# Optimization experiments

Measured on AMD Instinct MI355X. Metric: run time of the kernel, lower is better.

The kernel has to match this reference:

```python
import jax, jax.numpy as jnp
import numpy as np

# MLA dims (DeepSeek-V2-Lite-class)
B, S, D = 2, 2048, 2048
H = 16
NOPE, ROPE, VD = 128, 64, 128   # qk_nope_head_dim, qk_rope_head_dim, v_head_dim
KV_RANK, Q_RANK = 512, 1536
EPS = 1e-6
THETA = 10000.0


def setup_inputs() -> dict:
    key = jax.random.key(0)
    ks = jax.random.split(key, 8)

    def init(k, shape, fan_in):
        return jax.random.normal(k, shape, jnp.float32) * (fan_in ** -0.5)

    return {
        "x": jax.random.normal(ks[0], (B, S, D), jnp.float32),
        "w_dq": init(ks[1], (D, Q_RANK), D),
        "q_a_norm": jnp.ones((Q_RANK,), jnp.float32),
        "w_uq": init(ks[2], (Q_RANK, H * (NOPE + ROPE)), Q_RANK),
        "w_dkv": init(ks[3], (D, KV_RANK + ROPE), D),
        "kv_a_norm": jnp.ones((KV_RANK,), jnp.float32),
        "w_ukv": init(ks[4], (KV_RANK, H * (NOPE + VD)), KV_RANK),
        "w_o": init(ks[5], (H * VD, D), H * VD),
    }


def _rmsnorm(x, w):
    return x * jax.lax.rsqrt(jnp.mean(x * x, axis=-1, keepdims=True) + EPS) * w


def _rope(x):
    # x: [B, S, H', d] -> rotary on last dim (half-split style)
    d = x.shape[-1]
    inv = 1.0 / (THETA ** (jnp.arange(0, d, 2, dtype=jnp.float32) / d))
    ang = jnp.arange(x.shape[1], dtype=jnp.float32)[:, None] * inv[None, :]  # [S, d/2]
    cos = jnp.cos(ang)[None, :, None, :]
    sin = jnp.sin(ang)[None, :, None, :]
    x1, x2 = jnp.split(x, 2, axis=-1)
    return jnp.concatenate([x1 * cos - x2 * sin, x2 * cos + x1 * sin], axis=-1)


def reference(x, w_dq, q_a_norm, w_uq, w_dkv, kv_a_norm, w_ukv, w_o):
    # --- low-rank Q projection ---
    q = _rmsnorm(x @ w_dq, q_a_norm) @ w_uq          # [B,S,H*(NOPE+ROPE)]
    q = q.reshape(B, S, H, NOPE + ROPE)
    q_nope, q_pe = q[..., :NOPE], q[..., NOPE:]

    # --- latent (compressed) KV projection + shared decoupled-RoPE key ---
    ckv = x @ w_dkv                                   # [B,S,KV_RANK+ROPE]
    c_kv, k_pe = ckv[..., :KV_RANK], ckv[..., KV_RANK:]
    kv = (_rmsnorm(c_kv, kv_a_norm) @ w_ukv).reshape(B, S, H, NOPE + VD)
    k_nope, v = kv[..., :NOPE], kv[..., NOPE:]

    # --- decoupled RoPE on rope dims only ---
    q_pe = _rope(q_pe)                                # [B,S,H,ROPE]
    k_pe = _rope(k_pe[:, :, None, :])                 # [B,S,1,ROPE] shared across heads

    qf = jnp.concatenate([q_nope, q_pe], axis=-1)     # [B,S,H,NOPE+ROPE]
    kf = jnp.concatenate([k_nope, jnp.broadcast_to(k_pe, (B, S, H, ROPE))], axis=-1)

    # --- scaled dot-product attention with causal mask ---
    scale = 1.0 / jnp.sqrt(jnp.float32(NOPE + ROPE))
    scores = jnp.einsum("bqhd,bkhd->bhqk", qf * scale, kf)  # [B,H,S,S]
    causal = jnp.tril(jnp.ones((S, S), bool))
    scores = jnp.where(causal[None, None], scores, -1e9)
    w = jax.nn.softmax(scores, axis=-1)
    o = jnp.einsum("bhqk,bkhd->bqhd", w, v).reshape(B, S, H * VD)
    return o @ w_o                                    # [B,S,D]
```

## Files before the change

kernel.cpp:

```cpp
#include <hip/hip_runtime.h>
#include <hip/hip_bf16.h>
#include <math.h>

#define SS 2048
#define HH 16
#define EPSF 1e-6f
#define MR 4096
#define L2T 13.287712379549449f
#define ASCL (0.07216878364870322f * 1.4426950408889634f)

typedef unsigned short u16;
typedef unsigned int u32;
typedef __attribute__((ext_vector_type(8))) short bf8_t;
typedef __attribute__((ext_vector_type(4))) float f4_t;

__device__ inline u16 f2b(float f) {
    __hip_bfloat16 h = __float2bfloat16(f);
    return __builtin_bit_cast(u16, h);
}
__device__ inline float b2f(u16 x) {
    u32 v = (u32)x << 16;
    return __builtin_bit_cast(float, v);
}

#define GLD16(g, l) __builtin_amdgcn_global_load_lds( \
    (const __attribute__((address_space(1))) u32*)(g), \
    (__attribute__((address_space(3))) u32*)(l), 16, 0, 0)

#define MFMA16(a,b,c) __builtin_amdgcn_mfma_f32_16x16x32_bf16((a),(b),(c),0,0,0)

__global__ void prep_k(const float* __restrict__ x, u16* __restrict__ xb,
                       const float* __restrict__ w_dq, const float* __restrict__ w_dkv,
                       const float* __restrict__ w_uq, const float* __restrict__ w_ukv,
                       const float* __restrict__ w_o,
                       u16* __restrict__ wT1, u16* __restrict__ wTuq,
                       u16* __restrict__ wTukv, u16* __restrict__ wTo) {
    __shared__ float tt[32][33];
    int blk = blockIdx.x, tid = threadIdx.x;
    if (blk < 8192) {
        int i = blk * 256 + tid;
        float4 v = ((const float4*)x)[i];
        ushort4 o;
        o.x = f2b(v.x); o.y = f2b(v.y); o.z = f2b(v.z); o.w = f2b(v.w);
        *(ushort4*)(xb + (size_t)i * 4) = o;
        return;
    }
    blk -= 8192;
    const float* W; u16* dst; int K, N, Npad, nx;
    if (blk < 3072)       { W = w_dq;  dst = wT1;                      K = 2048; N = 1536; Npad = 1536; nx = 48; }
    else if (blk < 4352)  { blk -= 3072; W = w_dkv; dst = wT1 + (size_t)1536 * 2048; K = 2048; N = 576;  Npad = 640;  nx = 20; }
    else if (blk < 8960)  { blk -= 4352; W = w_uq;  dst = wTuq;        K = 1536; N = 3072; Npad = 3072; nx = 96; }
    else if (blk < 11008) { blk -= 8960; W = w_ukv; dst = wTukv;       K = 512;  N = 4096; Npad = 4096; nx = 128; }
    else                  { blk -= 11008; W = w_o;  dst = wTo;         K = 2048; N = 2048; Npad = 2048; nx = 64; }
    int n0 = (blk % nx) * 32, k0 = (blk / nx) * 32;
    int tx = tid & 31, ty = tid >> 5;
    for (int i = ty; i < 32; i += 8) {
        int n = n0 + tx;
        tt[i][tx] = (n < N) ? W[(size_t)(k0 + i) * N + n] : 0.f;
    }
    __syncthreads();
    for (int i = ty; i < 32; i += 8) {
        int n = n0 + i;
        if (n < Npad) dst[(size_t)n * K + k0 + tx] = f2b(tt[tx][i]);
    }
}

template <int MODE>
__global__ __launch_bounds__(256, 2)
void gemm_mfma(const u16* __restrict__ A, const u16* __restrict__ BT,
               void* __restrict__ Cv, int K, int N) {
    __shared__ u16 lA[128 * 32];
    __shared__ u16 lB[128 * 32];
    const int tid = threadIdx.x;
    const int w = tid >> 6, lane = tid & 63;
    const int quad = lane >> 4, col = lane & 15;
    const int wm = (w >> 1) * 64, wn = (w & 1) * 64;
    const int bm = blockIdx.y * 128, bn = blockIdx.x * 128;
    const int srow = lane >> 2;
    const int scol = (lane & 3) * 8;
    f4_t acc[4][4] = {};
    for (int k0 = 0; k0 < K; k0 += 32) {
        __syncthreads();
        #pragma unroll
        for (int cc = 0; cc < 2; cc++) {
            int c = 2 * w + cc;
            int row = c * 16 + srow;
            GLD16(A  + (size_t)(bm + row) * K + k0 + scol, (char*)lA + c * 1024);
            GLD16(BT + (size_t)(bn + row) * K + k0 + scol, (char*)lB + c * 1024);
        }
        __syncthreads();
        bf8_t af[4], bf[4];
        #pragma unroll
        for (int i = 0; i < 4; i++) {
            af[i] = *(const bf8_t*)(lA + (wm + i * 16 + col) * 32 + quad * 8);
            bf[i] = *(const bf8_t*)(lB + (wn + i * 16 + col) * 32 + quad * 8);
        }
        #pragma unroll
        for (int mi = 0; mi < 4; mi++)
            #pragma unroll
            for (int ni = 0; ni < 4; ni++)
                acc[mi][ni] = MFMA16(af[mi], bf[ni], acc[mi][ni]);
    }
    if (MODE == 0) {
        float* C = (float*)Cv;
        #pragma unroll
        for (int mi = 0; mi < 4; mi++)
            #pragma unroll
            for (int ni = 0; ni < 4; ni++) {
                int n = bn + wn + ni * 16 + col;
                #pragma unroll
                for (int r = 0; r < 4; r++) {
                    int m = bm + wm + mi * 16 + quad * 4 + r;
                    C[(size_t)m * N + n] = acc[mi][ni][r];
                }
            }
    } else if (MODE == 1) {
        u16* C = (u16*)Cv;
        #pragma unroll
        for (int mi = 0; mi < 4; mi++)
            #pragma unroll
            for (int ni = 0; ni < 4; ni++) {
                int n = bn + wn + ni * 16 + col;
                #pragma unroll
                for (int r = 0; r < 4; r++) {
                    int m = bm + wm + mi * 16 + quad * 4 + r;
                    C[(size_t)m * N + n] = f2b(acc[mi][ni][r]);
                }
            }
    } else {
        u16* C = (u16*)Cv;
        int span = ((bn + wn) >> 6) % 3;
        if (span < 2) {
            #pragma unroll
            for (int mi = 0; mi < 4; mi++)
                #pragma unroll
                for (int ni = 0; ni < 4; ni++) {
                    int n = bn + wn + ni * 16 + col;
                    #pragma unroll
                    for (int r = 0; r < 4; r++) {
                        int m = bm + wm + mi * 16 + quad * 4 + r;
                        C[(size_t)m * N + n] = f2b(acc[mi][ni][r] * ASCL);
                    }
                }
        } else {
            #pragma unroll
            for (int ni = 0; ni < 2; ni++) {
                int e = ni * 16 + col;
                float inv = exp2f(-(float)e * (L2T / 32.0f));
                #pragma unroll
                for (int mi = 0; mi < 4; mi++) {
                    #pragma unroll
                    for (int r = 0; r < 4; r++) {
                        int m = bm + wm + mi * 16 + quad * 4 + r;
                        int pos = m & (SS - 1);
                        float ang = (float)pos * inv;
                        float cs, sn; sincosf(ang, &sn, &cs);
                        float x1 = acc[mi][ni][r], x2 = acc[mi][ni + 2][r];
                        int n = bn + wn + ni * 16 + col;
                        C[(size_t)m * N + n]      = f2b((x1 * cs - x2 * sn) * ASCL);
                        C[(size_t)m * N + n + 32] = f2b((x2 * cs + x1 * sn) * ASCL);
                    }
                }
            }
        }
    }
}

__global__ void rmsq_k(const u16* __restrict__ C1, const float* __restrict__ wt,
                       u16* __restrict__ qlb) {
    __shared__ float red[256];
    int row = blockIdx.x, tid = threadIdx.x;
    const ushort4* rp = (const ushort4*)(C1 + (size_t)row * 2176);
    float s = 0.f;
    for (int i = tid; i < 384; i += 256) {
        ushort4 u = rp[i];
        float a = b2f(u.x), b = b2f(u.y), c = b2f(u.z), d = b2f(u.w);
        s += a * a + b * b + c * c + d * d;
    }
    red[tid] = s;
    __syncthreads();
    for (int off = 128; off > 0; off >>= 1) {
        if (tid < off) red[tid] += red[tid + off];
        __syncthreads();
    }
    float sc = rsqrtf(red[0] * (1.0f / 1536.0f) + EPSF);
    ushort4* op = (ushort4*)(qlb + (size_t)row * 1536);
    const float4* wv = (const float4*)wt;
    for (int i = tid; i < 384; i += 256) {
        ushort4 u = rp[i];
        float4 ww = wv[i];
        ushort4 o;
        o.x = f2b(b2f(u.x) * sc * ww.x);
        o.y = f2b(b2f(u.y) * sc * ww.y);
        o.z = f2b(b2f(u.z) * sc * ww.z);
        o.w = f2b(b2f(u.w) * sc * ww.w);
        op[i] = o;
    }
}

__global__ void rmskv_rope_k(const u16* __restrict__ C1, const float* __restrict__ wt,
                             u16* __restrict__ ckvnb, u16* __restrict__ kpeb) {
    __shared__ float red[256];
    int row = blockIdx.x, tid = threadIdx.x;
    const u16* base = C1 + (size_t)row * 2176 + 1536;
    if (tid < 32) {
        int t = tid;
        float x1 = b2f(base[512 + t]), x2 = b2f(base[544 + t]);
        int pos = row & (SS - 1);
        float inv = exp2f(-(float)t * (L2T / 32.0f));
        float ang = (float)pos * inv;
        float cs, sn; sincosf(ang, &sn, &cs);
        kpeb[(size_t)row * 64 + t]      = f2b(x1 * cs - x2 * sn);
        kpeb[(size_t)row * 64 + 32 + t] = f2b(x2 * cs + x1 * sn);
    }
    const ushort4* rp = (const ushort4*)base;
    float s = 0.f;
    if (tid < 128) {
        ushort4 u = rp[tid];
        float a = b2f(u.x), b = b2f(u.y), c = b2f(u.z), d = b2f(u.w);
        s = a * a + b * b + c * c + d * d;
    }
    red[tid] = s;
    __syncthreads();
    for (int off = 128; off > 0; off >>= 1) {
        if (tid < off) red[tid] += red[tid + off];
        __syncthreads();
    }
    float sc = rsqrtf(red[0] * (1.0f / 512.0f) + EPSF);
    if (tid < 128) {
        ushort4 u = rp[tid];
        float4 ww = ((const float4*)wt)[tid];
        ushort4 o;
        o.x = f2b(b2f(u.x) * sc * ww.x);
        o.y = f2b(b2f(u.y) * sc * ww.y);
        o.z = f2b(b2f(u.z) * sc * ww.z);
        o.w = f2b(b2f(u.w) * sc * ww.w);
        ((ushort4*)(ckvnb + (size_t)row * 512))[tid] = o;
    }
}

__global__ __launch_bounds__(256, 3)
void attn_mfma(const u16* __restrict__ qb, const u16* __restrict__ kvb,
               const u16* __restrict__ kpe, u16* __restrict__ ob) {
    __shared__ u16 lK[64 * 200];
    __shared__ u16 lV[128 * 72];
    __shared__ u16 lP[4 * 16 * 80];
    const int tid = threadIdx.x, w = tid >> 6, lane = tid & 63;
    const int quad = lane >> 4, col = lane & 15;
    const int bh = blockIdx.x, b = bh >> 4, h = bh & 15;
    const int tok0 = b * SS;
    int offE[7], isKV[7];
    #pragma unroll
    for (int jj = 0; jj < 7; jj++) {
        int c = w + 4 * jj;
        int o_b = c * 1024 + lane * 16;
        int row = o_b / 400;
        int ro = o_b - row * 400;
        if (ro < 256)      { offE[jj] = (row * 16 + h) * 256 + (ro >> 1); isKV[jj] = 1; }
        else if (ro < 384) { offE[jj] = row * 64 + ((ro - 256) >> 1);     isKV[jj] = 0; }
        else               { offE[jj] = 0;                                 isKV[jj] = 0; }
    }
    const int kp2 = lane & 31, dh = lane >> 5;
    u16* pw = lP + w * 16 * 80;

    for (int ph = 0; ph < 2; ph++) {
        const int qt = ph ? (31 - (int)blockIdx.y) : (int)blockIdx.y;
        bf8_t qf[6];
        {
            int qtok = tok0 + qt * 64 + w * 16 + col;
            const u16* qp = qb + ((size_t)qtok * HH + h) * 192 + quad * 8;
            #pragma unroll
            for (int kc = 0; kc < 6; kc++) qf[kc] = *(const bf8_t*)(qp + kc * 32);
        }
        f4_t o[8] = {};
        float mrow[4] = {-1e30f, -1e30f, -1e30f, -1e30f};
        float lrow[4] = {0.f, 0.f, 0.f, 0.f};
        for (int kt = 0; kt <= qt; kt++) {
            int ktok = tok0 + kt * 64;
            __syncthreads();
            #pragma unroll
            for (int jj = 0; jj < 7; jj++) {
                int c = w + 4 * jj;
                if (c < 25) {
                    const u16* src = isKV[jj] ? kvb + (size_t)ktok * 4096 + offE[jj]
                                              : kpe + (size_t)ktok * 64   + offE[jj];
                    GLD16(src, (char*)lK + c * 1024);
                }
            }
            #pragma unroll
            for (int i = 0; i < 2; i++) {
                int dv8 = w * 4 + dh * 2 + i;
                const u16* v0 = kvb + ((size_t)(ktok + 2 * kp2) * HH + h) * 256 + 128 + dv8 * 8;
                uint4 a4 = *(const uint4*)v0;
                uint4 b4 = *(const uint4*)(v0 + 4096);
                u32 av[4] = {a4.x, a4.y, a4.z, a4.w};
                u32 bv[4] = {b4.x, b4.y, b4.z, b4.w};
                u32* dst = (u32*)lV + (size_t)(dv8 * 8) * 36 + kp2;
                #pragma unroll
                for (int t = 0; t < 4; t++) {
                    u32 lo = __builtin_amdgcn_perm(bv[t], av[t], 0x05040100u);
                    u32 hi = __builtin_amdgcn_perm(bv[t], av[t], 0x07060302u);
                    dst[(2 * t) * 36]     = lo;
                    dst[(2 * t + 1) * 36] = hi;
                }
            }
            __syncthreads();
            bool diag = (kt == qt);
            f4_t s[4] = {};
            #pragma unroll
            for (int t = 0; t < 4; t++) {
                if (!diag || t <= w) {
                    #pragma unroll
                    for (int kc = 0; kc < 6; kc++) {
                        bf8_t kf = *(const bf8_t*)(lK + (t * 16 + col) * 200 + kc * 32 + quad * 8);
                        s[t] = MFMA16(qf[kc], kf, s[t]);
                    }
                }
            }
            if (diag) {
                #pragma unroll
                for (int t = 0; t < 4; t++) {
                    int kg = t * 16 + col;
                    #pragma unroll
                    for (int r = 0; r < 4; r++) {
                        int qg = w * 16 + quad * 4 + r;
                        if (kg > qg) s[t][r] = -1e30f;
                    }
                }
            }
            float sm[4] = {-1e30f, -1e30f, -1e30f, -1e30f};
            #pragma unroll
            for (int t = 0; t < 4; t++)
                #pragma unroll
                for (int r = 0; r < 4; r++) sm[r] = fmaxf(sm[r], s[t][r]);
            #pragma unroll
            for (int off = 1; off < 16; off <<= 1)
                #pragma unroll
                for (int r = 0; r < 4; r++) sm[r] = fmaxf(sm[r], __shfl_xor(sm[r], off));
            float al[4];
            #pragma unroll
            for (int r = 0; r < 4; r++) {
                float mn = fmaxf(mrow[r], sm[r]);
                al[r] = exp2f(mrow[r] - mn);
                mrow[r] = mn;
            }
            float rs[4] = {0.f, 0.f, 0.f, 0.f};
            #pragma unroll
            for (int t = 0; t < 4; t++)
                #pragma unroll
                for (int r = 0; r < 4; r++) {
                    float p = exp2f(s[t][r] - mrow[r]);
                    s[t][r] = p;
                    rs[r] += p;
                }
            #pragma unroll
            for (int off = 1; off < 16; off <<= 1)
                #pragma unroll
                for (int r = 0; r < 4; r++) rs[r] += __shfl_xor(rs[r], off);
            #pragma unroll
            for (int r = 0; r < 4; r++) lrow[r] = lrow[r] * al[r] + rs[r];
            #pragma unroll
            for (int n = 0; n < 8; n++)
                #pragma unroll
                for (int r = 0; r < 4; r++) o[n][r] *= al[r];
            #pragma unroll
            for (int t = 0; t < 4; t++)
                #pragma unroll
                for (int r = 0; r < 4; r++)
                    pw[(quad * 4 + r) * 80 + t * 16 + col] = f2b(s[t][r]);
            #pragma unroll
            for (int kc2 = 0; kc2 < 2; kc2++) {
                bf8_t pf = *(const bf8_t*)(pw + col * 80 + kc2 * 32 + quad * 8);
                #pragma unroll
                for (int n = 0; n < 8; n++) {
                    bf8_t vf = *(const bf8_t*)(lV + (n * 16 + col) * 72 + kc2 * 32 + quad * 8);
                    o[n] = MFMA16(pf, vf, o[n]);
                }
            }
        }
        #pragma unroll
        for (int n = 0; n < 8; n++)
            #pragma unroll
            for (int r = 0; r < 4; r++) {
                int qtok = tok0 + qt * 64 + w * 16 + quad * 4 + r;
                ob[((size_t)qtok * HH + h) * 128 + n * 16 + col] = f2b(o[n][r] / lrow[r]);
            }
    }
}

extern "C" void kernel_launch(void* const* d_in, const int* in_sizes, int n_in,
                              void* d_out, int out_size, void* d_ws, size_t ws_size,
                              hipStream_t stream) {
    const float* x        = (const float*)d_in[0];
    const float* w_dq     = (const float*)d_in[1];
    const float* q_a_norm = (const float*)d_in[2];
    const float* w_uq     = (const float*)d_in[3];
    const float* w_dkv    = (const float*)d_in[4];
    const float* kv_a_nrm = (const float*)d_in[5];
    const float* w_ukv    = (const float*)d_in[6];
    const float* w_o      = (const float*)d_in[7];
    float* out = (float*)d_out;

    char* ws = (char*)d_ws;
    const size_t MB = 1024 * 1024;
    u16* xb    = (u16*)(ws);
    u16* wT1   = (u16*)(ws + 17 * MB);
    u16* wTuq  = (u16*)(ws + 26 * MB);
    u16* wTukv = (u16*)(ws + 36 * MB);
    u16* wTo   = (u16*)(ws + 41 * MB);
    u16* C1    = (u16*)(ws + 50 * MB);
    u16* qlb   = (u16*)(ws + 68 * MB);
    u16* qbuf  = (u16*)(ws + 81 * MB);
    u16* ckvnb = (u16*)(ws + 106 * MB);
    u16* kpeb  = (u16*)(ws + 110 * MB);
    u16* kvb   = (u16*)(ws + 111 * MB);
    u16* aob   = xb;

    prep_k<<<23296, 256, 0, stream>>>(x, xb, w_dq, w_dkv, w_uq, w_ukv, w_o,
                                      wT1, wTuq, wTukv, wTo);
    gemm_mfma<1><<<dim3(17, 32), 256, 0, stream>>>(xb, wT1, C1, 2048, 2176);
    rmsq_k<<<MR, 256, 0, stream>>>(C1, q_a_norm, qlb);
    gemm_mfma<2><<<dim3(24, 32), 256, 0, stream>>>(qlb, wTuq, qbuf, 1536, 3072);
    rmskv_rope_k<<<MR, 256, 0, stream>>>(C1, kv_a_nrm, ckvnb, kpeb);
    gemm_mfma<1><<<dim3(32, 32), 256, 0, stream>>>(ckvnb, wTukv, kvb, 512, 4096);
    attn_mfma<<<dim3(32, 16), 256, 0, stream>>>(qbuf, kvb, kpeb, aob);
    gemm_mfma<0><<<dim3(16, 32), 256, 0, stream>>>(aob, wTo, out, 2048, 2048);
}
```

Before: 462.0 us.

## Restructure KV layout: head-major K with rope, transposed V, double-buffered attention

The up-projection GEMM epilogue now writes K as a per-token, per-head 192-wide buffer, with the shared rope key broadcast into it by a merged RMS-norm kernel. V is written transposed per head so attention can read V fragments straight from global memory into registers, with no LDS transpose. The attention kernel double-buffers K tiles in LDS, prefetching the next tile while computing the current one, and drops occupancy to 2. The two RMS kernels are merged into one launch and GEMM launch bounds are tuned per call; the cost is redundant K-rope storage and more global traffic for V.

```diff
diff --git a/kernel.cpp b/kernel.cpp
--- a/kernel.cpp
+++ b/kernel.cpp
@@ -65,10 +65,10 @@
     }
 }
 
-template <int MODE>
-__global__ __launch_bounds__(256, 2)
+template <int MODE, int MINW>
+__global__ __launch_bounds__(256, MINW)
 void gemm_mfma(const u16* __restrict__ A, const u16* __restrict__ BT,
-               void* __restrict__ Cv, int K, int N) {
+               void* __restrict__ Cv, void* __restrict__ Cv2, int K, int N) {
     __shared__ u16 lA[128 * 32];
     __shared__ u16 lB[128 * 32];
     const int tid = threadIdx.x;
@@ -127,7 +127,7 @@
                     C[(size_t)m * N + n] = f2b(acc[mi][ni][r]);
                 }
             }
-    } else {
+    } else if (MODE == 2) {
         u16* C = (u16*)Cv;
         int span = ((bn + wn) >> 6) % 3;
         if (span < 2) {
@@ -163,105 +163,138 @@
                 }
             }
         }
-    }
-}
-
-__global__ void rmsq_k(const u16* __restrict__ C1, const float* __restrict__ wt,
-                       u16* __restrict__ qlb) {
+    } else {
+        u16* kb = (u16*)Cv;
+        u16* vT = (u16*)Cv2;
+        #pragma unroll
+        for (int ni = 0; ni < 4; ni++) {
+            int nb = bn + wn + ni * 16;
+            int h = nb >> 8;
+            int cb = nb & 255;
+            if (cb < 128) {
+                #pragma unroll
+                for (int mi = 0; mi < 4; mi++)
+                    #pragma unroll
+                    for (int r = 0; r < 4; r++) {
+                        int m = bm + wm + mi * 16 + quad * 4 + r;
+                        kb[((size_t)m * HH + h) * 192 + cb + col] = f2b(acc[mi][ni][r]);
+                    }
+            } else {
+                int dv = cb - 128 + col;
+                #pragma unroll
+                for (int mi = 0; mi < 4; mi++) {
+                    int mb = bm + wm + mi * 16 + quad * 4;
+                    ushort4 o;
+                    o.x = f2b(acc[mi][ni][0]);
+                    o.y = f2b(acc[mi][ni][1]);
+                    o.z = f2b(acc[mi][ni][2]);
+                    o.w = f2b(acc[mi][ni][3]);
+                    *(ushort4*)(vT + ((size_t)h * 128 + dv) * 4096 + mb) = o;
+                }
+            }
+        }
+    }
+}
+
+__global__ void rms_all_k(const u16* __restrict__ C1, const float* __restrict__ wq,
+                          const float* __restrict__ wkv,
+                          u16* __restrict__ qlb, u16* __restrict__ ckvnb,
+                          u16* __restrict__ kb) {
     __shared__ float red[256];
-    int row = blockIdx.x, tid = threadIdx.x;
-    const ushort4* rp = (const ushort4*)(C1 + (size_t)row * 2176);
-    float s = 0.f;
-    for (int i = tid; i < 384; i += 256) {
-        ushort4 u = rp[i];
-        float a = b2f(u.x), b = b2f(u.y), c = b2f(u.z), d = b2f(u.w);
-        s += a * a + b * b + c * c + d * d;
-    }
-    red[tid] = s;
-    __syncthreads();
-    for (int off = 128; off > 0; off >>= 1) {
-        if (tid < off) red[tid] += red[tid + off];
+    int tid = threadIdx.x;
+    if (blockIdx.x < 4096) {
+        int row = blockIdx.x;
+        const ushort4* rp = (const ushort4*)(C1 + (size_t)row * 2176);
+        float s = 0.f;
+        for (int i = tid; i < 384; i += 256) {
+            ushort4 u = rp[i];
+            float a = b2f(u.x), b = b2f(u.y), c = b2f(u.z), d = b2f(u.w);
+            s += a * a + b * b + c * c + d * d;
+        }
+        red[tid] = s;
         __syncthreads();
-    }
-    float sc = rsqrtf(red[0] * (1.0f / 1536.0f) + EPSF);
-    ushort4* op = (ushort4*)(qlb + (size_t)row * 1536);
-    const float4* wv = (const float4*)wt;
-    for (int i = tid; i < 384; i += 256) {
-        ushort4 u = rp[i];
-        float4 ww = wv[i];
-        ushort4 o;
-        o.x = f2b(b2f(u.x) * sc * ww.x);
-        o.y = f2b(b2f(u.y) * sc * ww.y);
-        o.z = f2b(b2f(u.z) * sc * ww.z);
-        o.w = f2b(b2f(u.w) * sc * ww.w);
-        op[i] = o;
-    }
-}
-
-__global__ void rmskv_rope_k(const u16* __restrict__ C1, const float* __restrict__ wt,
-                             u16* __restrict__ ckvnb, u16* __restrict__ kpeb) {
-    __shared__ float red[256];
-    int row = blockIdx.x, tid = threadIdx.x;
-    const u16* base = C1 + (size_t)row * 2176 + 1536;
-    if (tid < 32) {
-        int t = tid;
-        float x1 = b2f(base[512 + t]), x2 = b2f(base[544 + t]);
-        int pos = row & (SS - 1);
-        float inv = exp2f(-(float)t * (L2T / 32.0f));
-        float ang = (float)pos * inv;
-        float cs, sn; sincosf(ang, &sn, &cs);
-        kpeb[(size_t)row * 64 + t]      = f2b(x1 * cs - x2 * sn);
-        kpeb[(size_t)row * 64 + 32 + t] = f2b(x2 * cs + x1 * sn);
-    }
-    const ushort4* rp = (const ushort4*)base;
-    float s = 0.f;
-    if (tid < 128) {
-        ushort4 u = rp[tid];
-        float a = b2f(u.x), b = b2f(u.y), c = b2f(u.z), d = b2f(u.w);
-        s = a * a + b * b + c * c + d * d;
-    }
-    red[tid] = s;
-    __syncthreads();
-    for (int off = 128; off > 0; off >>= 1) {
-        if (tid < off) red[tid] += red[tid + off];
+        for (int off = 128; off > 0; off >>= 1) {
+            if (tid < off) red[tid] += red[tid + off];
+            __syncthreads();
+        }
+        float sc = rsqrtf(red[0] * (1.0f / 1536.0f) + EPSF);
+        ushort4* op = (ushort4*)(qlb + (size_t)row * 1536);
+        const float4* wv = (const float4*)wq;
+        for (int i = tid; i < 384; i += 256) {
+            ushort4 u = rp[i];
+            float4 ww = wv[i];
+            ushort4 o;
+            o.x = f2b(b2f(u.x) * sc * ww.x);
+            o.y = f2b(b2f(u.y) * sc * ww.y);
+            o.z = f2b(b2f(u.z) * sc * ww.z);
+            o.w = f2b(b2f(u.w) * sc * ww.w);
+            op[i] = o;
+        }
+    } else {
+        int row = blockIdx.x - 4096;
+        const u16* base = C1 + (size_t)row * 2176 + 1536;
+        if (tid < 32) {
+            int t = tid;
+            float x1 = b2f(base[512 + t]), x2 = b2f(base[544 + t]);
+            int pos = row & (SS - 1);
+            float inv = exp2f(-(float)t * (L2T / 32.0f));
+            float ang = (float)pos * inv;
+            float cs, sn; sincosf(ang, &sn, &cs);
+            u16 y1 = f2b(x1 * cs - x2 * sn);
+            u16 y2 = f2b(x2 * cs + x1 * sn);
+            u16* kr = kb + (size_t)row * HH * 192;
+            #pragma unroll
+            for (int h = 0; h < HH; h++) {
+                kr[h * 192 + 128 + t] = y1;
+                kr[h * 192 + 160 + t] = y2;
+            }
+        }
+        const ushort4* rp = (const ushort4*)base;
+        float s = 0.f;
+        if (tid < 128) {
+            ushort4 u = rp[tid];
+            float a = b2f(u.x), b = b2f(u.y), c = b2f(u.z), d = b2f(u.w);
+            s = a * a + b * b + c * c + d * d;
+        }
+        red[tid] = s;
         __syncthreads();
-    }
-    float sc = rsqrtf(red[0] * (1.0f / 512.0f) + EPSF);
-    if (tid < 128) {
-        ushort4 u = rp[tid];
-        float4 ww = ((const float4*)wt)[tid];
-        ushort4 o;
-        o.x = f2b(b2f(u.x) * sc * ww.x);
-        o.y = f2b(b2f(u.y) * sc * ww.y);
-        o.z = f2b(b2f(u.z) * sc * ww.z);
-        o.w = f2b(b2f(u.w) * sc * ww.w);
-        ((ushort4*)(ckvnb + (size_t)row * 512))[tid] = o;
-    }
-}
-
-__global__ __launch_bounds__(256, 3)
-void attn_mfma(const u16* __restrict__ qb, const u16* __restrict__ kvb,
-               const u16* __restrict__ kpe, u16* __restrict__ ob) {
-    __shared__ u16 lK[64 * 200];
-    __shared__ u16 lV[128 * 72];
-    __shared__ u16 lP[4 * 16 * 80];
+        for (int off = 128; off > 0; off >>= 1) {
+            if (tid < off) red[tid] += red[tid + off];
+            __syncthreads();
+        }
+        float sc = rsqrtf(red[0] * (1.0f / 512.0f) + EPSF);
+        if (tid < 128) {
+            ushort4 u = rp[tid];
+            float4 ww = ((const float4*)wkv)[tid];
+            ushort4 o;
+            o.x = f2b(b2f(u.x) * sc * ww.x);
+            o.y = f2b(b2f(u.y) * sc * ww.y);
+            o.z = f2b(b2f(u.z) * sc * ww.z);
+            o.w = f2b(b2f(u.w) * sc * ww.w);
+            ((ushort4*)(ckvnb + (size_t)row * 512))[tid] = o;
+        }
+    }
+}
+
+__global__ __launch_bounds__(256, 2)
+void attn_mfma(const u16* __restrict__ qb, const u16* __restrict__ kb,
+               const u16* __restrict__ vT, u16* __restrict__ ob) {
+    __shared__ u16 lK[2][64 * 200];
+    __shared__ u16 lP[4 * 16 * 72];
     const int tid = threadIdx.x, w = tid >> 6, lane = tid & 63;
     const int quad = lane >> 4, col = lane & 15;
     const int bh = blockIdx.x, b = bh >> 4, h = bh & 15;
     const int tok0 = b * SS;
-    int offE[7], isKV[7];
+    int goff[7];
     #pragma unroll
     for (int jj = 0; jj < 7; jj++) {
         int c = w + 4 * jj;
         int o_b = c * 1024 + lane * 16;
         int row = o_b / 400;
         int ro = o_b - row * 400;
-        if (ro < 256)      { offE[jj] = (row * 16 + h) * 256 + (ro >> 1); isKV[jj] = 1; }
-        else if (ro < 384) { offE[jj] = row * 64 + ((ro - 256) >> 1);     isKV[jj] = 0; }
-        else               { offE[jj] = 0;                                 isKV[jj] = 0; }
-    }
-    const int kp2 = lane & 31, dh = lane >> 5;
-    u16* pw = lP + w * 16 * 80;
+        goff[jj] = (ro < 384) ? (row * HH + h) * 192 + (ro >> 1) : 0;
+    }
+    u16* pw = lP + w * 16 * 72;
 
     for (int ph = 0; ph < 2; ph++) {
         const int qt = ph ? (31 - (int)blockIdx.y) : (int)blockIdx.y;
@@ -275,36 +308,36 @@
         f4_t o[8] = {};
         float mrow[4] = {-1e30f, -1e30f, -1e30f, -1e30f};
         float lrow[4] = {0.f, 0.f, 0.f, 0.f};
-        for (int kt = 0; kt <= qt; kt++) {
-            int ktok = tok0 + kt * 64;
-            __syncthreads();
+        {
+            size_t kbase = (size_t)(tok0) * (HH * 192);
             #pragma unroll
             for (int jj = 0; jj < 7; jj++) {
                 int c = w + 4 * jj;
-                if (c < 25) {
-                    const u16* src = isKV[jj] ? kvb + (size_t)ktok * 4096 + offE[jj]
-                                              : kpe + (size_t)ktok * 64   + offE[jj];
-                    GLD16(src, (char*)lK + c * 1024);
-                }
-            }
-            #pragma unroll
-            for (int i = 0; i < 2; i++) {
-                int dv8 = w * 4 + dh * 2 + i;
-                const u16* v0 = kvb + ((size_t)(ktok + 2 * kp2) * HH + h) * 256 + 128 + dv8 * 8;
-                uint4 a4 = *(const uint4*)v0;
-                uint4 b4 = *(const uint4*)(v0 + 4096);
-                u32 av[4] = {a4.x, a4.y, a4.z, a4.w};
-                u32 bv[4] = {b4.x, b4.y, b4.z, b4.w};
-                u32* dst = (u32*)lV + (size_t)(dv8 * 8) * 36 + kp2;
-                #pragma unroll
-                for (int t = 0; t < 4; t++) {
-                    u32 lo = __builtin_amdgcn_perm(bv[t], av[t], 0x05040100u);
-                    u32 hi = __builtin_amdgcn_perm(bv[t], av[t], 0x07060302u);
-                    dst[(2 * t) * 36]     = lo;
-                    dst[(2 * t + 1) * 36] = hi;
-                }
-            }
-            __syncthreads();
+                if (c < 25) GLD16(kb + kbase + goff[jj], (char*)lK[0] + c * 1024);
+            }
+        }
+        __syncthreads();
+        for (int kt = 0; kt <= qt; kt++) {
+            const u16* cur = lK[kt & 1];
+            if (kt < qt) {
+                size_t kbase = (size_t)(tok0 + (kt + 1) * 64) * (HH * 192);
+                u16* nxt = (u16*)lK[(kt + 1) & 1];
+                #pragma unroll
+                for (int jj = 0; jj < 7; jj++) {
+                    int c = w + 4 * jj;
+                    if (c < 25) GLD16(kb + kbase + goff[jj], (char*)nxt + c * 1024);
+                }
+            }
+            bf8_t vf[2][8];
+            {
+                const u16* vbase = vT + (size_t)(h * 128 + col) * 4096
+                                 + tok0 + kt * 64 + quad * 8;
+                #pragma unroll
+                for (int kc2 = 0; kc2 < 2; kc2++)
+                    #pragma unroll
+                    for (int n = 0; n < 8; n++)
+                        vf[kc2][n] = *(const bf8_t*)(vbase + (size_t)(n * 16) * 4096 + kc2 * 32);
+            }
             bool diag = (kt == qt);
             f4_t s[4] = {};
             #pragma unroll
@@ -312,7 +345,7 @@
                 if (!diag || t <= w) {
                     #pragma unroll
                     for (int kc = 0; kc < 6; kc++) {
-                        bf8_t kf = *(const bf8_t*)(lK + (t * 16 + col) * 200 + kc * 32 + quad * 8);
+                        bf8_t kf = *(const bf8_t*)(cur + (t * 16 + col) * 200 + kc * 32 + quad * 8);
                         s[t] = MFMA16(qf[kc], kf, s[t]);
                     }
                 }
@@ -367,16 +400,15 @@
             for (int t = 0; t < 4; t++)
                 #pragma unroll
                 for (int r = 0; r < 4; r++)
-                    pw[(quad * 4 + r) * 80 + t * 16 + col] = f2b(s[t][r]);
+                    pw[(quad * 4 + r) * 72 + t * 16 + col] = f2b(s[t][r]);
             #pragma unroll
             for (int kc2 = 0; kc2 < 2; kc2++) {
-                bf8_t pf = *(const bf8_t*)(pw + col * 80 + kc2 * 32 + quad * 8);
-                #pragma unroll
-                for (int n = 0; n < 8; n++) {
-                    bf8_t vf = *(const bf8_t*)(lV + (n * 16 + col) * 72 + kc2 * 32 + quad * 8);
-                    o[n] = MFMA16(pf, vf, o[n]);
-                }
-            }
+                bf8_t pf = *(const bf8_t*)(pw + col * 72 + kc2 * 32 + quad * 8);
+                #pragma unroll
+                for (int n = 0; n < 8; n++)
+                    o[n] = MFMA16(pf, vf[kc2][n], o[n]);
+            }
+            __syncthreads();
         }
         #pragma unroll
         for (int n = 0; n < 8; n++)
@@ -411,18 +443,17 @@
     u16* C1    = (u16*)(ws + 50 * MB);
     u16* qlb   = (u16*)(ws + 68 * MB);
     u16* qbuf  = (u16*)(ws + 81 * MB);
-    u16* ckvnb = (u16*)(ws + 106 * MB);
-    u16* kpeb  = (u16*)(ws + 110 * MB);
-    u16* kvb   = (u16*)(ws + 111 * MB);
+    u16* ckvnb = (u16*)(ws + 107 * MB);
+    u16* kb    = (u16*)(ws + 112 * MB);
+    u16* vT    = (u16*)(ws + 138 * MB);
     u16* aob   = xb;
 
     prep_k<<<23296, 256, 0, stream>>>(x, xb, w_dq, w_dkv, w_uq, w_ukv, w_o,
                                       wT1, wTuq, wTukv, wTo);
-    gemm_mfma<1><<<dim3(17, 32), 256, 0, stream>>>(xb, wT1, C1, 2048, 2176);
-    rmsq_k<<<MR, 256, 0, stream>>>(C1, q_a_norm, qlb);
-    gemm_mfma<2><<<dim3(24, 32), 256, 0, stream>>>(qlb, wTuq, qbuf, 1536, 3072);
-    rmskv_rope_k<<<MR, 256, 0, stream>>>(C1, kv_a_nrm, ckvnb, kpeb);
-    gemm_mfma<1><<<dim3(32, 32), 256, 0, stream>>>(ckvnb, wTukv, kvb, 512, 4096);
-    attn_mfma<<<dim3(32, 16), 256, 0, stream>>>(qbuf, kvb, kpeb, aob);
-    gemm_mfma<0><<<dim3(16, 32), 256, 0, stream>>>(aob, wTo, out, 2048, 2048);
-}
+    gemm_mfma<1, 3><<<dim3(17, 32), 256, 0, stream>>>(xb, wT1, C1, nullptr, 2048, 2176);
+    rms_all_k<<<8192, 256, 0, stream>>>(C1, q_a_norm, kv_a_nrm, qlb, ckvnb, kb);
+    gemm_mfma<2, 2><<<dim3(24, 32), 256, 0, stream>>>(qlb, wTuq, qbuf, nullptr, 1536, 3072);
+    gemm_mfma<3, 3><<<dim3(32, 32), 256, 0, stream>>>(ckvnb, wTukv, kb, vT, 512, 4096);
+    attn_mfma<<<dim3(32, 16), 256, 0, stream>>>(qbuf, kb, vT, aob);
+    gemm_mfma<0, 3><<<dim3(16, 32), 256, 0, stream>>>(aob, wTo, out, nullptr, 2048, 2048);
+}
```

New measurement: 498.1 us. 7.8% more time.
